# Kernel tuning notes

Measured on AMD Instinct MI355X. Metric: run time of the kernel, lower is better.

Reference implementation:

```python
import jax, jax.numpy as jnp
import numpy as np

H = 512          # hidden_size
SF = 4           # scale_factor
B, S, L = 16, 2048, 2

def setup_inputs() -> dict:
    key = jax.random.key(0)
    ks = jax.random.split(key, 9)
    return {
        "hidden": jax.random.normal(ks[0], (L, B, H * SF), dtype=jnp.float32),
        "encoder_outputs": jax.random.normal(ks[1], (B, S, H * SF), dtype=jnp.float32),
        "We": jax.random.normal(ks[2], (H, H * SF), dtype=jnp.float32) * 0.02,
        "be": jax.random.normal(ks[3], (H,), dtype=jnp.float32) * 0.02,
        "Wh": jax.random.normal(ks[4], (H, H * SF), dtype=jnp.float32) * 0.02,
        "bh": jax.random.normal(ks[5], (H,), dtype=jnp.float32) * 0.02,
        "Wa": jax.random.normal(ks[6], (H, 2 * H), dtype=jnp.float32) * 0.02,
        "ba": jax.random.normal(ks[7], (H,), dtype=jnp.float32) * 0.02,
        "v": jax.random.uniform(ks[8], (1, H), dtype=jnp.float32),
    }

def reference(hidden, encoder_outputs, We, be, Wh, bh, Wa, ba, v):
    # hidden[-1]: [B, 4H] -> [B, H]
    h = hidden[-1] @ Wh.T + bh
    # encoder_outputs: [B, S, 4H] -> [B, S, H]
    eo = jnp.einsum('bsf,hf->bsh', encoder_outputs, We) + be
    # concat([h broadcast to S, eo]) @ Wa.T == h @ Wa_h.T + eo @ Wa_e.T (split concat matmul)
    Wa_h, Wa_e = Wa[:, :H], Wa[:, H:]
    energy = jnp.tanh(h[:, None, :] @ Wa_h.T + jnp.einsum('bsh,kh->bsk', eo, Wa_e) + ba)  # [B,S,H]
    scores = jnp.einsum('bsh,h->bs', energy, v[0])           # [B,S]
    attn_weights = jax.nn.softmax(scores, axis=1)            # [B,S]
    context_vector = jnp.einsum('bs,bsh->bh', attn_weights, eo)  # [B,H]
    return (context_vector, attn_weights)
```

## Files before the change

kernel.cpp:

```cpp
#include <hip/hip_runtime.h>
#include <math.h>

#define HH 512
#define FF 2048
#define BB 16
#define SS 2048
#define MM 32768

using f32x4 = __attribute__((ext_vector_type(4))) float;
using s16x8 = __attribute__((ext_vector_type(8))) short;

struct __align__(8)  US4 { unsigned short x, y, z, w; };
struct __align__(16) US8 { unsigned short s[8]; };

__device__ __forceinline__ unsigned short f2bf(float f) {
  unsigned int u = __builtin_bit_cast(unsigned int, f);
  u += 0x7fffu + ((u >> 16) & 1u);
  return (unsigned short)(u >> 16);
}
__device__ __forceinline__ float bf2f(unsigned short u) {
  unsigned int x = ((unsigned int)u) << 16;
  return __builtin_bit_cast(float, x);
}
__device__ __forceinline__ void gload_lds16(const void* g, void* l) {
  __builtin_amdgcn_global_load_lds(
      (const __attribute__((address_space(1))) unsigned int*)g,
      (__attribute__((address_space(3))) unsigned int*)l, 16, 0, 0);
}

__global__ void k_conv(const float* __restrict__ We, const float* __restrict__ Wa,
                       unsigned short* __restrict__ OWe, unsigned short* __restrict__ OWa) {
  int bid = blockIdx.x, t = threadIdx.x;
  if (bid < 1024) {
    int idx = bid * 256 + t;
    f32x4 x = *(const f32x4*)(We + (size_t)idx * 4);
    US4 p{f2bf(x.x), f2bf(x.y), f2bf(x.z), f2bf(x.w)};
    *(US4*)(OWe + (size_t)idx * 4) = p;
  } else {
    int idx = (bid - 1024) * 256 + t;
    int k = idx >> 7, h4 = idx & 127;
    f32x4 x = *(const f32x4*)(Wa + (size_t)k * 1024 + 512 + h4 * 4);
    US4 p{f2bf(x.x), f2bf(x.y), f2bf(x.z), f2bf(x.w)};
    *(US4*)(OWa + (size_t)idx * 4) = p;
  }
}

__global__ void k_h(const float* __restrict__ hidden, const float* __restrict__ Wh,
                    const float* __restrict__ bh, float* __restrict__ h_ws) {
  int t = threadIdx.x, lane = t & 63, wid = t >> 6;
  int out = blockIdx.x * 4 + wid;
  int b = out >> 9, j = out & 511;
  const float* hr = hidden + (1) * BB * FF + b * FF;
  const float* wr = Wh + (size_t)j * FF;
  float a = 0.f;
#pragma unroll
  for (int i = 0; i < 8; ++i) {
    int o = i * 256 + lane * 4;
    f32x4 x = *(const f32x4*)(hr + o);
    f32x4 y = *(const f32x4*)(wr + o);
    a += x.x * y.x + x.y * y.y + x.z * y.z + x.w * y.w;
  }
#pragma unroll
  for (int m = 32; m; m >>= 1) a += __shfl_xor(a, m);
  if (lane == 0) h_ws[out] = a + bh[j];
}

__global__ void k_bb(const float* __restrict__ h_ws, const float* __restrict__ Wa,
                     const float* __restrict__ ba, float* __restrict__ bb_ws) {
  int t = threadIdx.x, lane = t & 63, wid = t >> 6;
  int out = blockIdx.x * 4 + wid;
  int b = out >> 9, k = out & 511;
  const float* hr = h_ws + b * HH;
  const float* wa = Wa + (size_t)k * 1024;
  float a = 0.f;
#pragma unroll
  for (int i = 0; i < 2; ++i) {
    int o = i * 256 + lane * 4;
    f32x4 x = *(const f32x4*)(hr + o);
    f32x4 y = *(const f32x4*)(wa + o);
    a += x.x * y.x + x.y * y.y + x.z * y.z + x.w * y.w;
  }
#pragma unroll
  for (int m = 32; m; m >>= 1) a += __shfl_xor(a, m);
  if (lane == 0) bb_ws[out] = a + ba[k];
}


template<int CUR, bool IB, bool IA, int WN>
__device__ __forceinline__ void gstep(const float* enc_m0, const unsigned short* Web,
                                      unsigned short* smem, int kt, int t, int lane, int wid,
                                      f32x4* regC, f32x4* regN, f32x4 (&acc)[4][4]) {
  unsigned short* Asc = smem + (CUR ? 4096 : 0);
  unsigned short* Asn = smem + (CUR ? 0 : 4096);
  unsigned short* Bsc = smem + (CUR ? 40960 : 8192);
  unsigned short* Bsn = smem + (CUR ? 8192 : 40960);
  asm volatile("s_waitcnt vmcnt(%0)" :: "i"(WN) : "memory");
  __builtin_amdgcn_sched_barrier(0);
  __builtin_amdgcn_s_barrier();
  if (IB) {
#pragma unroll
    for (int i = 0; i < 8; ++i) {
      int idx = i * 512 + t, row = idx >> 3, c = idx & 7, sc = c ^ (row & 7);
      gload_lds16(Web + (size_t)row * FF + (kt + 64) + sc * 8, Bsn + idx * 8);
    }
  }
  __builtin_amdgcn_sched_barrier(0);
  if (IA) {
#pragma unroll
    for (int i = 0; i < 2; ++i) {
      int idx = i * 512 + t, row = idx >> 4, c4 = idx & 15;
      regN[i] = *(const f32x4*)(enc_m0 + (size_t)row * FF + (kt + 128) + c4 * 4);
    }
  }
  __builtin_amdgcn_sched_barrier(0);
#pragma unroll
  for (int ks = 0; ks < 2; ++ks) {
    s16x8 af[4], bfr[4];
#pragma unroll
    for (int mi = 0; mi < 4; ++mi) {
      int row = mi * 16 + (lane & 15);
      int byte = row * 128 + (((ks * 64) + (lane >> 4) * 16) ^ ((row & 7) << 4));
      af[mi] = *(const s16x8*)((const char*)Asc + byte);
    }
#pragma unroll
    for (int ni = 0; ni < 4; ++ni) {
      int row = wid * 64 + ni * 16 + (lane & 15);
      int byte = row * 128 + (((ks * 64) + (lane >> 4) * 16) ^ ((row & 7) << 4));
      bfr[ni] = *(const s16x8*)((const char*)Bsc + byte);
    }
#pragma unroll
    for (int mi = 0; mi < 4; ++mi)
#pragma unroll
      for (int ni = 0; ni < 4; ++ni)
        acc[mi][ni] = __builtin_amdgcn_mfma_f32_16x16x32_bf16(af[mi], bfr[ni], acc[mi][ni], 0, 0, 0);
  }
  if (IB) {
#pragma unroll
    for (int i = 0; i < 2; ++i) {
      int idx = i * 512 + t, row = idx >> 4, c4 = idx & 15;
      f32x4 x = regC[i];
      US4 p{f2bf(x.x), f2bf(x.y), f2bf(x.z), f2bf(x.w)};
      int byte = row * 128 + ((c4 * 8) ^ ((row & 7) << 4));
      *(US4*)((char*)Asn + byte) = p;
    }
  }
  asm volatile("s_waitcnt lgkmcnt(0)" ::: "memory");
  __builtin_amdgcn_sched_barrier(0);
  __builtin_amdgcn_s_barrier();
}

__global__ __launch_bounds__(512, 2) void k_gemm1f(
    const float* __restrict__ enc, const unsigned short* __restrict__ Web,
    const float* __restrict__ be, const unsigned short* __restrict__ Waeb,
    const float* __restrict__ bbw, const float* __restrict__ vv,
    unsigned short* __restrict__ eo, float* __restrict__ sp) {
  __shared__ unsigned short smem[73728];
  const int t = threadIdx.x, lane = t & 63, wid = t >> 6;
  const int m0 = blockIdx.x * 64;
  const float* enc_m0 = enc + (size_t)m0 * FF;
  unsigned short* As0 = smem;
  unsigned short* Bs0 = smem + 8192;
  f32x4 acc[4][4] = {};
  f32x4 areg0[2], areg1[2], aP[2];

#pragma unroll
  for (int i = 0; i < 2; ++i) {
    int idx = i * 512 + t, row = idx >> 4, c4 = idx & 15;
    aP[i] = *(const f32x4*)(enc_m0 + (size_t)row * FF + c4 * 4);
  }
  __builtin_amdgcn_sched_barrier(0);
#pragma unroll
  for (int i = 0; i < 8; ++i) {
    int idx = i * 512 + t, row = idx >> 3, c = idx & 7, sc = c ^ (row & 7);
    gload_lds16(Web + (size_t)row * FF + sc * 8, Bs0 + idx * 8);
  }
  __builtin_amdgcn_sched_barrier(0);
#pragma unroll
  for (int i = 0; i < 2; ++i) {
    int idx = i * 512 + t, row = idx >> 4, c4 = idx & 15;
    areg1[i] = *(const f32x4*)(enc_m0 + (size_t)row * FF + 64 + c4 * 4);
  }
  __builtin_amdgcn_sched_barrier(0);
#pragma unroll
  for (int i = 0; i < 2; ++i) {
    int idx = i * 512 + t, row = idx >> 4, c4 = idx & 15;
    f32x4 x = aP[i];
    US4 p{f2bf(x.x), f2bf(x.y), f2bf(x.z), f2bf(x.w)};
    int byte = row * 128 + ((c4 * 8) ^ ((row & 7) << 4));
    *(US4*)((char*)As0 + byte) = p;
  }
  asm volatile("s_waitcnt lgkmcnt(0)" ::: "memory");
  __builtin_amdgcn_sched_barrier(0);
  __builtin_amdgcn_s_barrier();

  int kt = 0;
#pragma unroll 1
  for (int tt = 0; tt < 15; ++tt) {
    gstep<0, true, true, 2>(enc_m0, Web, smem, kt, t, lane, wid, areg1, areg0, acc);
    gstep<1, true, true, 2>(enc_m0, Web, smem, kt + 64, t, lane, wid, areg0, areg1, acc);
    kt += 128;
  }
  gstep<0, true, false, 2>(enc_m0, Web, smem, 1920, t, lane, wid, areg1, areg0, acc);
  gstep<1, false, false, 0>(enc_m0, Web, smem, 1984, t, lane, wid, areg0, areg1, acc);

  unsigned short* Cs = smem + 40960;
#pragma unroll
  for (int ni = 0; ni < 4; ++ni) {
    int col = wid * 64 + ni * 16 + (lane & 15);
    float bev = be[col];
#pragma unroll
    for (int mi = 0; mi < 4; ++mi)
#pragma unroll
      for (int j = 0; j < 4; ++j) {
        int row = mi * 16 + (lane >> 4) * 4 + j;
        int byte = row * 1024 + ((col * 2) ^ ((row & 7) << 4));
        *(unsigned short*)((char*)Cs + byte) = f2bf(acc[mi][ni][j] + bev);
      }
  }
  __syncthreads();

#pragma unroll
  for (int i = 0; i < 8; ++i) {
    int idx = i * 512 + t, row = idx >> 6, c = idx & 63;
    int byte = row * 1024 + ((c * 16) ^ ((row & 7) << 4));
    *(US8*)(eo + (size_t)(m0 + row) * HH + c * 8) = *(const US8*)((const char*)Cs + byte);
  }

  f32x4 acc2[4][4] = {};
#pragma unroll 1
  for (int kt2 = 0; kt2 < HH; kt2 += 64) {
#pragma unroll
    for (int ks = 0; ks < 2; ++ks) {
      int k2 = kt2 + ks * 32 + (lane >> 4) * 8;
      s16x8 af[4], bfr[4];
#pragma unroll
      for (int mi = 0; mi < 4; ++mi) {
        int row = mi * 16 + (lane & 15);
        int byte = row * 1024 + ((k2 * 2) ^ ((row & 7) << 4));
        af[mi] = *(const s16x8*)((const char*)Cs + byte);
      }
#pragma unroll
      for (int ni = 0; ni < 4; ++ni) {
        int nrow = wid * 64 + ni * 16 + (lane & 15);
        bfr[ni] = *(const s16x8*)(Waeb + (size_t)nrow * HH + k2);
      }
#pragma unroll
      for (int mi = 0; mi < 4; ++mi)
#pragma unroll
        for (int ni = 0; ni < 4; ++ni)
          acc2[mi][ni] = __builtin_amdgcn_mfma_f32_16x16x32_bf16(af[mi], bfr[ni], acc2[mi][ni], 0, 0, 0);
    }
  }

  const int b = m0 >> 11;
  float vcol[4], bcol[4];
#pragma unroll
  for (int ni = 0; ni < 4; ++ni) {
    int col = wid * 64 + ni * 16 + (lane & 15);
    vcol[ni] = vv[col];
    bcol[ni] = bbw[b * HH + col];
  }
  float ps[4][4];
#pragma unroll
  for (int mi = 0; mi < 4; ++mi)
#pragma unroll
    for (int j = 0; j < 4; ++j) {
      float s = 0.f;
#pragma unroll
      for (int ni = 0; ni < 4; ++ni)
        s += tanhf(acc2[mi][ni][j] + bcol[ni]) * vcol[ni];
      ps[mi][j] = s;
    }
#pragma unroll
  for (int m = 1; m < 16; m <<= 1)
#pragma unroll
    for (int mi = 0; mi < 4; ++mi)
#pragma unroll
      for (int j = 0; j < 4; ++j) ps[mi][j] += __shfl_xor(ps[mi][j], m);
  float* red = (float*)smem;
  if ((lane & 15) == 0) {
#pragma unroll
    for (int mi = 0; mi < 4; ++mi)
#pragma unroll
      for (int j = 0; j < 4; ++j)
        red[wid * 64 + mi * 16 + (lane >> 4) * 4 + j] = ps[mi][j];
  }
  __syncthreads();
  if (t < 64) {
    float s = 0.f;
#pragma unroll
    for (int w = 0; w < 8; ++w) s += red[w * 64 + t];
    sp[m0 + t] = s;
  }
}

__global__ void k_softmax(const float* __restrict__ sp, float* __restrict__ attn) {
  const int b = blockIdx.x, t = threadIdx.x, lane = t & 63, wid = t >> 6;
  __shared__ float red[4];
  float vals[8], lmax = -3.0e38f;
#pragma unroll
  for (int i = 0; i < 8; ++i) {
    float x = sp[b * SS + t + i * 256];
    vals[i] = x;
    lmax = fmaxf(lmax, x);
  }
#pragma unroll
  for (int m = 32; m; m >>= 1) lmax = fmaxf(lmax, __shfl_xor(lmax, m));
  if (lane == 0) red[wid] = lmax;
  __syncthreads();
  lmax = fmaxf(fmaxf(red[0], red[1]), fmaxf(red[2], red[3]));
  __syncthreads();
  float lsum = 0.f;
#pragma unroll
  for (int i = 0; i < 8; ++i) {
    vals[i] = __expf(vals[i] - lmax);
    lsum += vals[i];
  }
#pragma unroll
  for (int m = 32; m; m >>= 1) lsum += __shfl_xor(lsum, m);
  if (lane == 0) red[wid] = lsum;
  __syncthreads();
  float inv = 1.0f / (red[0] + red[1] + red[2] + red[3]);
#pragma unroll
  for (int i = 0; i < 8; ++i) attn[b * SS + t + i * 256] = vals[i] * inv;
}

__global__ __launch_bounds__(512) void k_ctx1(const unsigned short* __restrict__ eo,
                                              const float* __restrict__ attn,
                                              float* __restrict__ cp) {
  __shared__ float red[8][512];
  const int b = blockIdx.x >> 4, ch = blockIdx.x & 15, t = threadIdx.x;
  const int tg = t & 63, sg = t >> 6;
  const float* aw = attn + b * SS + ch * 128;
  float acc[8] = {};
#pragma unroll 4
  for (int i = 0; i < 16; ++i) {
    int s = sg + i * 8;
    float w = aw[s];
    US8 vv8 = *(const US8*)(eo + (size_t)(b * SS + ch * 128 + s) * HH + tg * 8);
#pragma unroll
    for (int j = 0; j < 8; ++j) acc[j] += w * bf2f(vv8.s[j]);
  }
#pragma unroll
  for (int j = 0; j < 8; ++j) red[sg][tg * 8 + j] = acc[j];
  __syncthreads();
  float a = 0.f;
#pragma unroll
  for (int g = 0; g < 8; ++g) a += red[g][t];
  cp[(size_t)blockIdx.x * HH + t] = a;
}

__global__ void k_ctx2(const float* __restrict__ cp, float* __restrict__ ctx) {
  const int b = blockIdx.x, h = threadIdx.x;
  float a = 0.f;
#pragma unroll
  for (int c = 0; c < 16; ++c) a += cp[(size_t)(b * 16 + c) * HH + h];
  ctx[b * HH + h] = a;
}

extern "C" void kernel_launch(void* const* d_in, const int* in_sizes, int n_in,
                              void* d_out, int out_size, void* d_ws, size_t ws_size,
                              hipStream_t stream) {
  (void)in_sizes; (void)n_in; (void)out_size; (void)ws_size;
  const float* hidden = (const float*)d_in[0];
  const float* enc    = (const float*)d_in[1];
  const float* We     = (const float*)d_in[2];
  const float* be     = (const float*)d_in[3];
  const float* Wh     = (const float*)d_in[4];
  const float* bh     = (const float*)d_in[5];
  const float* Wa     = (const float*)d_in[6];
  const float* ba     = (const float*)d_in[7];
  const float* v      = (const float*)d_in[8];

  float* out  = (float*)d_out;
  float* ctx  = out;
  float* attn = out + BB * HH;

  char* ws = (char*)d_ws;
  unsigned short* Web  = (unsigned short*)ws;  ws += (size_t)HH * FF * 2;
  unsigned short* Waeb = (unsigned short*)ws;  ws += (size_t)HH * HH * 2;
  float* h_ws  = (float*)ws;                   ws += (size_t)BB * HH * 4;
  float* bb_ws = (float*)ws;                   ws += (size_t)BB * HH * 4;
  unsigned short* eo = (unsigned short*)ws;    ws += (size_t)MM * HH * 2;
  float* sp = (float*)ws;                      ws += (size_t)MM * 4;
  float* cp = (float*)ws;                      ws += (size_t)BB * 16 * HH * 4;

  k_conv<<<1280, 256, 0, stream>>>(We, Wa, Web, Waeb);
  k_h<<<2048, 256, 0, stream>>>(hidden, Wh, bh, h_ws);
  k_bb<<<2048, 256, 0, stream>>>(h_ws, Wa, ba, bb_ws);
  k_gemm1f<<<512, 512, 0, stream>>>(enc, Web, be, Waeb, bb_ws, v, eo, sp);
  k_softmax<<<16, 256, 0, stream>>>(sp, attn);
  k_ctx1<<<256, 512, 0, stream>>>(eo, attn, cp);
  k_ctx2<<<16, 512, 0, stream>>>(cp, ctx);
}
```

Measured before the change: 187.3 us.

## Replace double-buffered GEMM pipeline with single-buffered loop for higher occupancy

Removes the templated double-buffered gstep pipeline (two A/B LDS buffers, explicit vmcnt waits and raw barriers) and uses a simple single-buffered K loop with __syncthreads around each tile. LDS use is halved and launch bounds are raised from 2 to 4 blocks per CU, so more blocks can be resident and hide latency. In exchange, a block no longer overlaps its global loads with its own MFMA work. The barriers likely wait on the prefetched A registers as well. The tighter register budget may also cause spills.

```diff
diff --git a/kernel.cpp b/kernel.cpp
--- a/kernel.cpp
+++ b/kernel.cpp
@@ -85,125 +85,75 @@
   if (lane == 0) bb_ws[out] = a + ba[k];
 }
 
-
-template<int CUR, bool IB, bool IA, int WN>
-__device__ __forceinline__ void gstep(const float* enc_m0, const unsigned short* Web,
-                                      unsigned short* smem, int kt, int t, int lane, int wid,
-                                      f32x4* regC, f32x4* regN, f32x4 (&acc)[4][4]) {
-  unsigned short* Asc = smem + (CUR ? 4096 : 0);
-  unsigned short* Asn = smem + (CUR ? 0 : 4096);
-  unsigned short* Bsc = smem + (CUR ? 40960 : 8192);
-  unsigned short* Bsn = smem + (CUR ? 8192 : 40960);
-  asm volatile("s_waitcnt vmcnt(%0)" :: "i"(WN) : "memory");
-  __builtin_amdgcn_sched_barrier(0);
-  __builtin_amdgcn_s_barrier();
-  if (IB) {
-#pragma unroll
-    for (int i = 0; i < 8; ++i) {
-      int idx = i * 512 + t, row = idx >> 3, c = idx & 7, sc = c ^ (row & 7);
-      gload_lds16(Web + (size_t)row * FF + (kt + 64) + sc * 8, Bsn + idx * 8);
-    }
-  }
-  __builtin_amdgcn_sched_barrier(0);
-  if (IA) {
-#pragma unroll
-    for (int i = 0; i < 2; ++i) {
-      int idx = i * 512 + t, row = idx >> 4, c4 = idx & 15;
-      regN[i] = *(const f32x4*)(enc_m0 + (size_t)row * FF + (kt + 128) + c4 * 4);
-    }
-  }
-  __builtin_amdgcn_sched_barrier(0);
-#pragma unroll
-  for (int ks = 0; ks < 2; ++ks) {
-    s16x8 af[4], bfr[4];
-#pragma unroll
-    for (int mi = 0; mi < 4; ++mi) {
-      int row = mi * 16 + (lane & 15);
-      int byte = row * 128 + (((ks * 64) + (lane >> 4) * 16) ^ ((row & 7) << 4));
-      af[mi] = *(const s16x8*)((const char*)Asc + byte);
-    }
-#pragma unroll
-    for (int ni = 0; ni < 4; ++ni) {
-      int row = wid * 64 + ni * 16 + (lane & 15);
-      int byte = row * 128 + (((ks * 64) + (lane >> 4) * 16) ^ ((row & 7) << 4));
-      bfr[ni] = *(const s16x8*)((const char*)Bsc + byte);
-    }
-#pragma unroll
-    for (int mi = 0; mi < 4; ++mi)
-#pragma unroll
-      for (int ni = 0; ni < 4; ++ni)
-        acc[mi][ni] = __builtin_amdgcn_mfma_f32_16x16x32_bf16(af[mi], bfr[ni], acc[mi][ni], 0, 0, 0);
-  }
-  if (IB) {
-#pragma unroll
-    for (int i = 0; i < 2; ++i) {
-      int idx = i * 512 + t, row = idx >> 4, c4 = idx & 15;
-      f32x4 x = regC[i];
-      US4 p{f2bf(x.x), f2bf(x.y), f2bf(x.z), f2bf(x.w)};
-      int byte = row * 128 + ((c4 * 8) ^ ((row & 7) << 4));
-      *(US4*)((char*)Asn + byte) = p;
-    }
-  }
-  asm volatile("s_waitcnt lgkmcnt(0)" ::: "memory");
-  __builtin_amdgcn_sched_barrier(0);
-  __builtin_amdgcn_s_barrier();
-}
-
-__global__ __launch_bounds__(512, 2) void k_gemm1f(
+__global__ __launch_bounds__(512, 4) void k_gemm1f(
     const float* __restrict__ enc, const unsigned short* __restrict__ Web,
     const float* __restrict__ be, const unsigned short* __restrict__ Waeb,
     const float* __restrict__ bbw, const float* __restrict__ vv,
     unsigned short* __restrict__ eo, float* __restrict__ sp) {
-  __shared__ unsigned short smem[73728];
+  __shared__ unsigned short smem[36864];
+  unsigned short* As = smem;
+  unsigned short* Bs = smem + 4096;
   const int t = threadIdx.x, lane = t & 63, wid = t >> 6;
   const int m0 = blockIdx.x * 64;
   const float* enc_m0 = enc + (size_t)m0 * FF;
-  unsigned short* As0 = smem;
-  unsigned short* Bs0 = smem + 8192;
   f32x4 acc[4][4] = {};
-  f32x4 areg0[2], areg1[2], aP[2];
-
+
+  f32x4 areg[2];
 #pragma unroll
   for (int i = 0; i < 2; ++i) {
     int idx = i * 512 + t, row = idx >> 4, c4 = idx & 15;
-    aP[i] = *(const f32x4*)(enc_m0 + (size_t)row * FF + c4 * 4);
-  }
-  __builtin_amdgcn_sched_barrier(0);
-#pragma unroll
-  for (int i = 0; i < 8; ++i) {
-    int idx = i * 512 + t, row = idx >> 3, c = idx & 7, sc = c ^ (row & 7);
-    gload_lds16(Web + (size_t)row * FF + sc * 8, Bs0 + idx * 8);
-  }
-  __builtin_amdgcn_sched_barrier(0);
-#pragma unroll
-  for (int i = 0; i < 2; ++i) {
-    int idx = i * 512 + t, row = idx >> 4, c4 = idx & 15;
-    areg1[i] = *(const f32x4*)(enc_m0 + (size_t)row * FF + 64 + c4 * 4);
-  }
-  __builtin_amdgcn_sched_barrier(0);
-#pragma unroll
-  for (int i = 0; i < 2; ++i) {
-    int idx = i * 512 + t, row = idx >> 4, c4 = idx & 15;
-    f32x4 x = aP[i];
-    US4 p{f2bf(x.x), f2bf(x.y), f2bf(x.z), f2bf(x.w)};
-    int byte = row * 128 + ((c4 * 8) ^ ((row & 7) << 4));
-    *(US4*)((char*)As0 + byte) = p;
-  }
-  asm volatile("s_waitcnt lgkmcnt(0)" ::: "memory");
-  __builtin_amdgcn_sched_barrier(0);
-  __builtin_amdgcn_s_barrier();
-
-  int kt = 0;
+    areg[i] = *(const f32x4*)(enc_m0 + (size_t)row * FF + c4 * 4);
+  }
+
 #pragma unroll 1
-  for (int tt = 0; tt < 15; ++tt) {
-    gstep<0, true, true, 2>(enc_m0, Web, smem, kt, t, lane, wid, areg1, areg0, acc);
-    gstep<1, true, true, 2>(enc_m0, Web, smem, kt + 64, t, lane, wid, areg0, areg1, acc);
-    kt += 128;
-  }
-  gstep<0, true, false, 2>(enc_m0, Web, smem, 1920, t, lane, wid, areg1, areg0, acc);
-  gstep<1, false, false, 0>(enc_m0, Web, smem, 1984, t, lane, wid, areg0, areg1, acc);
-
-  unsigned short* Cs = smem + 40960;
+  for (int kt = 0; kt < FF; kt += 64) {
+#pragma unroll
+    for (int i = 0; i < 8; ++i) {
+      int idx = i * 512 + t, row = idx >> 3, c = idx & 7, sc = c ^ (row & 7);
+      gload_lds16(Web + (size_t)row * FF + kt + sc * 8, Bs + idx * 8);
+    }
+#pragma unroll
+    for (int i = 0; i < 2; ++i) {
+      int idx = i * 512 + t, row = idx >> 4, c4 = idx & 15;
+      f32x4 x = areg[i];
+      US4 p{f2bf(x.x), f2bf(x.y), f2bf(x.z), f2bf(x.w)};
+      int byte = row * 128 + ((c4 * 8) ^ ((row & 7) << 4));
+      *(US4*)((char*)As + byte) = p;
+    }
+    {
+      int ktn = (kt + 64 < FF) ? kt + 64 : 0;
+#pragma unroll
+      for (int i = 0; i < 2; ++i) {
+        int idx = i * 512 + t, row = idx >> 4, c4 = idx & 15;
+        areg[i] = *(const f32x4*)(enc_m0 + (size_t)row * FF + ktn + c4 * 4);
+      }
+    }
+    __syncthreads();
+#pragma unroll
+    for (int ks = 0; ks < 2; ++ks) {
+      s16x8 af[4], bfr[4];
+#pragma unroll
+      for (int mi = 0; mi < 4; ++mi) {
+        int row = mi * 16 + (lane & 15);
+        int byte = row * 128 + (((ks * 64) + (lane >> 4) * 16) ^ ((row & 7) << 4));
+        af[mi] = *(const s16x8*)((const char*)As + byte);
+      }
+#pragma unroll
+      for (int ni = 0; ni < 4; ++ni) {
+        int row = wid * 64 + ni * 16 + (lane & 15);
+        int byte = row * 128 + (((ks * 64) + (lane >> 4) * 16) ^ ((row & 7) << 4));
+        bfr[ni] = *(const s16x8*)((const char*)Bs + byte);
+      }
+#pragma unroll
+      for (int mi = 0; mi < 4; ++mi)
+#pragma unroll
+        for (int ni = 0; ni < 4; ++ni)
+          acc[mi][ni] = __builtin_amdgcn_mfma_f32_16x16x32_bf16(af[mi], bfr[ni], acc[mi][ni], 0, 0, 0);
+    }
+    __syncthreads();
+  }
+
+  unsigned short* Cs = smem + 4096;
 #pragma unroll
   for (int ni = 0; ni < 4; ++ni) {
     int col = wid * 64 + ni * 16 + (lane & 15);
```

Result: faster. 168.8 us (-9.9%).
